# Performance work log

Hardware: AMD Instinct MI355X
Metric: run time of the kernel (lower is better)

## Reference

```python
import jax, jax.numpy as jnp
import numpy as np

EPS = 1e-3
D_MODEL = 512
SEQ = 1024
BATCH = 4
N_LAYERS = 2
N_HEAD = 8
D_HEAD = 64
D_INNER = 1024


def _position_table(n_pos, d):
    # Faithful to PositionEncoding: sin applied to even cols; the cos line in
    # the source is a no-op (missing assignment), so odd cols stay raw.
    j = np.arange(d)
    pos = np.arange(n_pos)[:, None]
    pe = pos / np.power(10000.0, 2 * (j // 2) / d)
    pe[0] = 0.0
    pe[1:, 0::2] = np.sin(pe[1:, 0::2])
    return jnp.asarray(pe, dtype=jnp.float32)


def _layer_norm(z, a, b):
    # torch.std is unbiased (ddof=1); eps added to sigma, not variance
    mu = jnp.mean(z, axis=-1, keepdims=True)
    sigma = jnp.sqrt(jnp.sum((z - mu) ** 2, axis=-1, keepdims=True) / (z.shape[-1] - 1))
    return (z - mu) / (sigma + EPS) * a + b


def setup_inputs() -> dict:
    key = jax.random.key(0)
    ks = jax.random.split(key, 10)
    s = 0.02
    return {
        "x": jax.random.normal(ks[0], (BATCH, SEQ, D_MODEL), dtype=jnp.float32),
        "pos_enc": _position_table(SEQ, D_MODEL),
        "w_qs": jax.random.normal(ks[1], (N_LAYERS, N_HEAD, D_MODEL, D_HEAD), dtype=jnp.float32) * s,
        "w_ks": jax.random.normal(ks[2], (N_LAYERS, N_HEAD, D_MODEL, D_HEAD), dtype=jnp.float32) * s,
        "w_vs": jax.random.normal(ks[3], (N_LAYERS, N_HEAD, D_MODEL, D_HEAD), dtype=jnp.float32) * s,
        "ln1_a": jnp.ones((N_LAYERS, D_MODEL), dtype=jnp.float32),
        "ln1_b": jnp.zeros((N_LAYERS, D_MODEL), dtype=jnp.float32),
        "w1": jax.random.normal(ks[4], (N_LAYERS, D_INNER, D_MODEL), dtype=jnp.float32) * s,
        "b1": jax.random.normal(ks[5], (N_LAYERS, D_INNER), dtype=jnp.float32) * s,
        "w2": jax.random.normal(ks[6], (N_LAYERS, D_MODEL, D_INNER), dtype=jnp.float32) * s,
        "b2": jax.random.normal(ks[7], (N_LAYERS, D_MODEL), dtype=jnp.float32) * s,
        "ln2_a": jnp.ones((N_LAYERS, D_MODEL), dtype=jnp.float32),
        "ln2_b": jnp.zeros((N_LAYERS, D_MODEL), dtype=jnp.float32),
    }


def reference(x, pos_enc, w_qs, w_ks, w_vs, ln1_a, ln1_b, w1, b1, w2, b2, ln2_a, ln2_b):
    temper = jnp.sqrt(jnp.float32(D_MODEL))  # scale uses d_model, not d_k (as in source)
    x = x + pos_enc[None, :, :]
    for i in range(N_LAYERS):
        residual = x
        # per-head projections: [h, b, l, dk]
        q = jnp.einsum('bld,hdk->hblk', x, w_qs[i])
        k = jnp.einsum('bld,hdk->hblk', x, w_ks[i])
        v = jnp.einsum('bld,hdv->hblv', x, w_vs[i])
        attn = jax.nn.softmax(jnp.einsum('hbqk,hbmk->hbqm', q, k) / temper, axis=-1)
        out = jnp.einsum('hbqm,hbmv->hbqv', attn, v)
        # permute(1,2,0,3): concat heads along feature dim -> [b, l, h*dv]
        out = out.transpose(1, 2, 0, 3).reshape(BATCH, SEQ, N_HEAD * D_HEAD)
        x = _layer_norm(out + residual, ln1_a[i], ln1_b[i])
        # positionwise FFN (1x1 convs == linears)
        h = jax.nn.relu(jnp.einsum('bld,fd->blf', x, w1[i]) + b1[i])
        o = jnp.einsum('blf,df->bld', h, w2[i]) + b2[i]
        x = _layer_norm(o + x, ln2_a[i], ln2_b[i])
    return x
```

## Files before the change

### kernel.cpp

```cpp
#include <hip/hip_runtime.h>
#include <math.h>

#define D_MODEL 512
#define SEQ     1024
#define BATCH   4
#define N_LAYERS 2
#define N_HEAD  8
#define D_HEAD  64
#define D_INNER 1024
#define NTOK    (BATCH*SEQ)
#define LN_EPS  1e-3f

typedef float f32x4 __attribute__((ext_vector_type(4)));
typedef short bf16x8 __attribute__((ext_vector_type(8)));
typedef unsigned short ushort_t;
typedef unsigned int uint_t;
typedef unsigned long long ull_t;

__device__ inline ushort_t f2bf(float f) {
    uint_t u = __float_as_uint(f);
    u += 0x7FFFu + ((u >> 16) & 1u);
    return (ushort_t)(u >> 16);
}
__device__ inline float bf2f(ushort_t h) {
    return __uint_as_float((uint_t)h << 16);
}

#define PREP_E0 (NTOK * D_MODEL)
#define PREP_E1 (1536 * 512)
#define PREP_EW (N_LAYERS * D_INNER * D_MODEL)
#define PREP_TOTAL (PREP_E0 + 2 * PREP_E1 + 2 * PREP_EW)

__global__ void prep_kernel(const float* __restrict__ x,
                            const float* __restrict__ pe,
                            const float* __restrict__ w_qs,
                            const float* __restrict__ w_ks,
                            const float* __restrict__ w_vs,
                            const float* __restrict__ w1,
                            const float* __restrict__ w2,
                            float* __restrict__ X,
                            ushort_t* __restrict__ Xraw,
                            ushort_t* __restrict__ Wqkv,
                            ushort_t* __restrict__ WqkvL,
                            ushort_t* __restrict__ W1b,
                            ushort_t* __restrict__ W2b) {
    int idx = blockIdx.x * 256 + threadIdx.x;
    if (idx < PREP_E0) {
        int l = (idx / D_MODEL) % SEQ;
        int d = idx % D_MODEL;
        float xv = x[idx];
        X[idx] = xv + pe[l * D_MODEL + d];
        Xraw[idx] = f2bf(xv);
        return;
    }
    idx -= PREP_E0;
    if (idx < 2 * PREP_E1) {
        int layer = idx / PREP_E1;
        int j = idx - layer * PREP_E1;
        int n = j >> 9, k = j & 511;
        int which = n >> 9, h = (n >> 6) & 7, d = n & 63;
        size_t wofs = (size_t)layer * N_HEAD * D_MODEL * D_HEAD;
        const float* W = (which == 0) ? w_qs + wofs
                       : (which == 1) ? w_ks + wofs : w_vs + wofs;
        float v = W[((size_t)h * D_MODEL + k) * D_HEAD + d];
        ushort_t hv = f2bf(v);
        Wqkv[(size_t)layer * PREP_E1 + j] = hv;
        if (layer == 0) WqkvL[j] = f2bf(v - bf2f(hv));
        return;
    }
    idx -= 2 * PREP_E1;
    if (idx < PREP_EW) { W1b[idx] = f2bf(w1[idx]); return; }
    idx -= PREP_EW;
    W2b[idx] = f2bf(w2[idx]);
}

__device__ inline void qkv_scatter(f32x4 a, int n, int m_base,
                                   const float* __restrict__ pew,
                                   ushort_t* Qhi, ushort_t* Qlo,
                                   ushort_t* Khi, ushort_t* Klo,
                                   ushort_t* Vt) {
    int which = n >> 9, hd = n & 511;
    int head = hd >> 6, d = hd & 63;
    int hb = head * BATCH + (m_base >> 10);
    int l  = m_base & 1023;
    if (pew) {
#pragma unroll
        for (int r = 0; r < 4; r++) a[r] += pew[(size_t)(l + r) * 1536 + n];
    }
    if (which == 2) {
        ushort4 pk = make_ushort4(f2bf(a[0]), f2bf(a[1]), f2bf(a[2]), f2bf(a[3]));
        *(ushort4*)(Vt + ((size_t)hb * D_HEAD + d) * SEQ + l) = pk;
    } else {
        ushort_t* H = (which == 0) ? Qhi : Khi;
        ushort_t* L = (which == 0) ? Qlo : Klo;
#pragma unroll
        for (int r = 0; r < 4; r++) {
            float v = a[r];
            ushort_t hv = f2bf(v);
            size_t off = ((size_t)hb * SEQ + l + r) * D_HEAD + d;
            H[off] = hv;
            L[off] = f2bf(v - bf2f(hv));
        }
    }
}

template<int MODE, int TM, int TN, int BK>
__global__ __launch_bounds__(256, 4)
void gemm_kernel(const ushort_t* __restrict__ A, const ushort_t* __restrict__ Bt,
                 const float* __restrict__ bias, const float* __restrict__ pew,
                 float* __restrict__ outF, ushort_t* __restrict__ outB,
                 ushort_t* __restrict__ Qhi, ushort_t* __restrict__ Qlo,
                 ushort_t* __restrict__ Khi, ushort_t* __restrict__ Klo,
                 ushort_t* __restrict__ Vt,
                 int M, int N, int K) {
    constexpr int WM = TM / 2, WN = TN / 2;
    constexpr int MT = WM / 16, NT = WN / 16;
    constexpr int CPR = BK / 8;
    __shared__ ushort_t As[TM][BK + 8];
    __shared__ ushort_t Bs[TN][BK + 8];
    const int tid = threadIdx.x;
    const int m0 = blockIdx.y * TM, n0 = blockIdx.x * TN;
    const int w = tid >> 6, lane = tid & 63;
    const int wr = w >> 1, wc = w & 1;
    const int col = lane & 15, quad = lane >> 4;

    f32x4 acc[MT][NT] = {};

    for (int k0 = 0; k0 < K; k0 += BK) {
        __syncthreads();
#pragma unroll
        for (int p = 0; p < TM * CPR / 256; p++) {
            int idx = p * 256 + tid;
            int row = idx / CPR, ch = (idx % CPR) * 8;
            *(uint4*)(&As[row][ch]) =
                *(const uint4*)(A + (size_t)(m0 + row) * K + k0 + ch);
        }
#pragma unroll
        for (int p = 0; p < TN * CPR / 256; p++) {
            int idx = p * 256 + tid;
            int row = idx / CPR, ch = (idx % CPR) * 8;
            *(uint4*)(&Bs[row][ch]) =
                *(const uint4*)(Bt + (size_t)(n0 + row) * K + k0 + ch);
        }
        __syncthreads();
#pragma unroll
        for (int ks = 0; ks < BK; ks += 32) {
            bf16x8 af[MT], bfr[NT];
#pragma unroll
            for (int t = 0; t < MT; t++)
                af[t] = *(const bf16x8*)(&As[wr * WM + t * 16 + col][ks + quad * 8]);
#pragma unroll
            for (int t = 0; t < NT; t++)
                bfr[t] = *(const bf16x8*)(&Bs[wc * WN + t * 16 + col][ks + quad * 8]);
#pragma unroll
            for (int mt = 0; mt < MT; mt++)
#pragma unroll
                for (int nt = 0; nt < NT; nt++)
                    acc[mt][nt] = __builtin_amdgcn_mfma_f32_16x16x32_bf16(
                        af[mt], bfr[nt], acc[mt][nt], 0, 0, 0);
        }
    }

#pragma unroll
    for (int mt = 0; mt < MT; mt++) {
#pragma unroll
        for (int nt = 0; nt < NT; nt++) {
            int n = n0 + wc * WN + nt * 16 + col;
            int m_base = m0 + wr * WM + mt * 16 + quad * 4;
            if (MODE == 0) {
                qkv_scatter(acc[mt][nt], n, m_base, pew, Qhi, Qlo, Khi, Klo, Vt);
            } else {
#pragma unroll
                for (int r = 0; r < 4; r++) {
                    int m = m_base + r;
                    float v = acc[mt][nt][r];
                    if (MODE == 1) {
                        float t = fmaxf(v + bias[n], 0.f);
                        outB[(size_t)m * N + n] = f2bf(t);
                    } else {
                        outF[(size_t)m * N + n] = v + bias[n];
                    }
                }
            }
        }
    }
}

__global__ __launch_bounds__(256, 4)
void gemm_hilo_kernel(const float* __restrict__ A,
                      const ushort_t* __restrict__ Bh,
                      const ushort_t* __restrict__ Bl,
                      float* __restrict__ outF, int M, int N, int K) {
    __shared__ ushort_t Ash[64][72];
    __shared__ ushort_t Asl[64][72];
    __shared__ ushort_t Bsh[64][72];
    __shared__ ushort_t Bsl[64][72];
    const int tid = threadIdx.x;
    const int m0 = blockIdx.y * 64, n0 = blockIdx.x * 64;
    const int w = tid >> 6, lane = tid & 63;
    const int wm = (w >> 1) * 32, wn = (w & 1) * 32;
    const int col = lane & 15, quad = lane >> 4;

    f32x4 acc[2][2] = {};

    for (int k0 = 0; k0 < K; k0 += 64) {
        __syncthreads();
#pragma unroll
        for (int p = 0; p < 4; p++) {
            int idx = p * 256 + tid;
            int row = idx >> 4, c4 = (idx & 15) * 4;
            float4 v = *(const float4*)(A + (size_t)(m0 + row) * K + k0 + c4);
            ushort_t h0 = f2bf(v.x), h1 = f2bf(v.y), h2 = f2bf(v.z), h3 = f2bf(v.w);
            *(ushort4*)(&Ash[row][c4]) = make_ushort4(h0, h1, h2, h3);
            *(ushort4*)(&Asl[row][c4]) = make_ushort4(
                f2bf(v.x - bf2f(h0)), f2bf(v.y - bf2f(h1)),
                f2bf(v.z - bf2f(h2)), f2bf(v.w - bf2f(h3)));
        }
#pragma unroll
        for (int p = 0; p < 2; p++) {
            int idx = p * 256 + tid;
            int row = idx >> 3, ch = (idx & 7) * 8;
            *(uint4*)(&Bsh[row][ch]) =
                *(const uint4*)(Bh + (size_t)(n0 + row) * K + k0 + ch);
            *(uint4*)(&Bsl[row][ch]) =
                *(const uint4*)(Bl + (size_t)(n0 + row) * K + k0 + ch);
        }
        __syncthreads();
#pragma unroll
        for (int ks = 0; ks < 64; ks += 32) {
            bf16x8 ah[2], al[2], bh[2], bl[2];
#pragma unroll
            for (int t = 0; t < 2; t++) {
                ah[t] = *(const bf16x8*)(&Ash[wm + t * 16 + col][ks + quad * 8]);
                al[t] = *(const bf16x8*)(&Asl[wm + t * 16 + col][ks + quad * 8]);
                bh[t] = *(const bf16x8*)(&Bsh[wn + t * 16 + col][ks + quad * 8]);
                bl[t] = *(const bf16x8*)(&Bsl[wn + t * 16 + col][ks + quad * 8]);
            }
#pragma unroll
            for (int mt = 0; mt < 2; mt++)
#pragma unroll
                for (int nt = 0; nt < 2; nt++) {
                    acc[mt][nt] = __builtin_amdgcn_mfma_f32_16x16x32_bf16(
                        ah[mt], bh[nt], acc[mt][nt], 0, 0, 0);
                    acc[mt][nt] = __builtin_amdgcn_mfma_f32_16x16x32_bf16(
                        ah[mt], bl[nt], acc[mt][nt], 0, 0, 0);
                    acc[mt][nt] = __builtin_amdgcn_mfma_f32_16x16x32_bf16(
                        al[mt], bh[nt], acc[mt][nt], 0, 0, 0);
                }
        }
    }

#pragma unroll
    for (int mt = 0; mt < 2; mt++)
#pragma unroll
        for (int nt = 0; nt < 2; nt++) {
            int n = n0 + wn + nt * 16 + col;
#pragma unroll
            for (int r = 0; r < 4; r++) {
                int m = m0 + wm + mt * 16 + quad * 4 + r;
                outF[(size_t)m * N + n] = acc[mt][nt][r];
            }
        }
}

template<bool HILO>
__global__ __launch_bounds__(256, 4)
void attention_kernel(const ushort_t* __restrict__ Qhi,
                      const ushort_t* __restrict__ Qlo,
                      const ushort_t* __restrict__ Khi,
                      const ushort_t* __restrict__ Klo,
                      const ushort_t* __restrict__ Vt,
                      float* __restrict__ P0,
                      float* __restrict__ P1,
                      float2* __restrict__ ML) {
    const int bid = blockIdx.x;
    const int split = bid >> 9;
    const int r9  = bid & 511;
    const int j   = r9 >> 3;
    const int hb  = (r9 & 7) * 4 + (j >> 4);
    const int qt  = j & 15;
    const int h = hb >> 2, b = hb & 3;
    const int tid = threadIdx.x;
    const int w = tid >> 6, lane = tid & 63;
    const int col = lane & 15, quad = lane >> 4;
    const size_t kbase = (size_t)hb * SEQ * D_HEAD;
    const size_t vbase = (size_t)hb * D_HEAD * SEQ;

    __shared__ ushort_t Kh[64][72];
    __shared__ ushort_t Kl[HILO ? 64 : 1][72];
    __shared__ ushort_t Vs[64][72];
    __shared__ ushort_t Pl[4][16][72];

    bf16x8 qh[2], ql[2];
    {
        const ushort_t* qp = Qhi + kbase + (size_t)(qt * 64 + w * 16 + col) * D_HEAD;
        qh[0] = *(const bf16x8*)(qp + quad * 8);
        qh[1] = *(const bf16x8*)(qp + 32 + quad * 8);
        if (HILO) {
            const ushort_t* lp = Qlo + kbase + (size_t)(qt * 64 + w * 16 + col) * D_HEAD;
            ql[0] = *(const bf16x8*)(lp + quad * 8);
            ql[1] = *(const bf16x8*)(lp + 32 + quad * 8);
        }
    }

    f32x4 acco[4] = {};
    float mrun = -1e30f, lrun = 0.f;
    const float inv_temper = 0.04419417382415922f;

    const int tbeg = split * (SEQ / 2);
    for (int t0 = tbeg; t0 < tbeg + SEQ / 2; t0 += 64) {
        __syncthreads();
#pragma unroll
        for (int p = 0; p < 2; p++) {
            int idx = p * 256 + tid;
            int row = idx >> 3, ch = (idx & 7) * 8;
            *(uint4*)(&Kh[row][ch]) =
                *(const uint4*)(Khi + kbase + (size_t)(t0 + row) * D_HEAD + ch);
            if (HILO)
                *(uint4*)(&Kl[row][ch]) =
                    *(const uint4*)(Klo + kbase + (size_t)(t0 + row) * D_HEAD + ch);
            *(uint4*)(&Vs[row][ch]) =
                *(const uint4*)(Vt + vbase + (size_t)row * SEQ + t0 + ch);
        }
        __syncthreads();

        float sc[4][4];
#pragma unroll
        for (int nt = 0; nt < 4; nt++) {
            bf16x8 kh0 = *(const bf16x8*)(&Kh[nt * 16 + col][quad * 8]);
            bf16x8 kh1 = *(const bf16x8*)(&Kh[nt * 16 + col][32 + quad * 8]);
            f32x4 s = {};
            s = __builtin_amdgcn_mfma_f32_16x16x32_bf16(kh0, qh[0], s, 0, 0, 0);
            s = __builtin_amdgcn_mfma_f32_16x16x32_bf16(kh1, qh[1], s, 0, 0, 0);
            if (HILO) {
                bf16x8 kl0 = *(const bf16x8*)(&Kl[nt * 16 + col][quad * 8]);
                bf16x8 kl1 = *(const bf16x8*)(&Kl[nt * 16 + col][32 + quad * 8]);
                s = __builtin_amdgcn_mfma_f32_16x16x32_bf16(kl0, qh[0], s, 0, 0, 0);
                s = __builtin_amdgcn_mfma_f32_16x16x32_bf16(kl1, qh[1], s, 0, 0, 0);
                s = __builtin_amdgcn_mfma_f32_16x16x32_bf16(kh0, ql[0], s, 0, 0, 0);
                s = __builtin_amdgcn_mfma_f32_16x16x32_bf16(kh1, ql[1], s, 0, 0, 0);
            }
#pragma unroll
            for (int r = 0; r < 4; r++) sc[nt][r] = s[r] * inv_temper;
        }

        bf16x8 va0[4], va1[4];
#pragma unroll
        for (int nt = 0; nt < 4; nt++) {
            va0[nt] = *(const bf16x8*)(&Vs[nt * 16 + col][quad * 8]);
            va1[nt] = *(const bf16x8*)(&Vs[nt * 16 + col][32 + quad * 8]);
        }

        float tmax = sc[0][0];
#pragma unroll
        for (int nt = 0; nt < 4; nt++)
#pragma unroll
            for (int r = 0; r < 4; r++) tmax = fmaxf(tmax, sc[nt][r]);
        tmax = fmaxf(tmax, __shfl_xor(tmax, 16, 64));
        tmax = fmaxf(tmax, __shfl_xor(tmax, 32, 64));

        float mn = fmaxf(mrun, tmax);
        float alpha = __expf(mrun - mn);
        mrun = mn;
        float tsum = 0.f;
#pragma unroll
        for (int nt = 0; nt < 4; nt++) {
            float p0 = __expf(sc[nt][0] - mn);
            float p1 = __expf(sc[nt][1] - mn);
            float p2 = __expf(sc[nt][2] - mn);
            float p3 = __expf(sc[nt][3] - mn);
            tsum += (p0 + p1) + (p2 + p3);
            ull_t pk = (ull_t)f2bf(p0) | ((ull_t)f2bf(p1) << 16)
                     | ((ull_t)f2bf(p2) << 32) | ((ull_t)f2bf(p3) << 48);
            *(ull_t*)(&Pl[w][col][nt * 16 + quad * 4]) = pk;
        }
        tsum += __shfl_xor(tsum, 16, 64);
        tsum += __shfl_xor(tsum, 32, 64);
        lrun = lrun * alpha + tsum;
#pragma unroll
        for (int nt = 0; nt < 4; nt++)
#pragma unroll
            for (int r = 0; r < 4; r++) acco[nt][r] *= alpha;

        __threadfence_block();

        union { ulong2 u; bf16x8 v; } pa0, pa1;
        pa0.u = *(const ulong2*)(&Pl[w][col][quad * 8]);
        pa1.u = *(const ulong2*)(&Pl[w][col][32 + quad * 8]);
#pragma unroll
        for (int nt = 0; nt < 4; nt++) {
            acco[nt] = __builtin_amdgcn_mfma_f32_16x16x32_bf16(va0[nt], pa0.v, acco[nt], 0, 0, 0);
            acco[nt] = __builtin_amdgcn_mfma_f32_16x16x32_bf16(va1[nt], pa1.v, acco[nt], 0, 0, 0);
        }
    }

    const int qrow = qt * 64 + w * 16 + col;
    float* dst = split ? P1 : P0;
#pragma unroll
    for (int nt = 0; nt < 4; nt++)
        *(f32x4*)(&dst[((size_t)b * SEQ + qrow) * D_MODEL + h * D_HEAD
                       + nt * 16 + quad * 4]) = acco[nt];
    if (quad == 0)
        ML[((size_t)split * 32 + hb) * SEQ + qrow] = make_float2(mrun, lrun);
}

__device__ inline float block_sum_256(float v, float* tmp) {
#pragma unroll
    for (int off = 32; off > 0; off >>= 1) v += __shfl_down(v, off, 64);
    if ((threadIdx.x & 63) == 0) tmp[threadIdx.x >> 6] = v;
    __syncthreads();
    return tmp[0] + tmp[1] + tmp[2] + tmp[3];
}

__global__ void add_norm_kernel(const float* __restrict__ A,
                                const float* __restrict__ R,
                                const float* __restrict__ ga,
                                const float* __restrict__ gb,
                                float* __restrict__ Out,
                                ushort_t* __restrict__ OutBf) {
    int tok = blockIdx.x, tid = threadIdx.x;
    __shared__ float t1[4], t2[4];
    size_t base = (size_t)tok * D_MODEL;
    float z0 = A[base + tid]       + R[base + tid];
    float z1 = A[base + tid + 256] + R[base + tid + 256];
    float s = block_sum_256(z0 + z1, t1);
    float mu = s * (1.f / (float)D_MODEL);
    float d0 = z0 - mu, d1 = z1 - mu;
    float ss = block_sum_256(d0 * d0 + d1 * d1, t2);
    float sigma = sqrtf(ss * (1.f / (float)(D_MODEL - 1)));
    float inv = 1.f / (sigma + LN_EPS);
    float r0 = d0 * inv * ga[tid]       + gb[tid];
    float r1 = d1 * inv * ga[tid + 256] + gb[tid + 256];
    Out[base + tid]         = r0;
    Out[base + tid + 256]   = r1;
    OutBf[base + tid]       = f2bf(r0);
    OutBf[base + tid + 256] = f2bf(r1);
}

__global__ void add_norm_combine_kernel(const float* __restrict__ Pa,
                                        const float* __restrict__ Pb,
                                        const float2* __restrict__ ML,
                                        const float* __restrict__ R,
                                        const float* __restrict__ ga,
                                        const float* __restrict__ gb,
                                        float* __restrict__ Out,
                                        ushort_t* __restrict__ OutBf) {
    int tok = blockIdx.x, tid = threadIdx.x;
    int b = tok >> 10, l = tok & 1023;
    __shared__ float t1[4], t2[4];
    int h0 = tid >> 6;
    float s0a, s0b, s1a, s1b;
    {
        int hb0 = h0 * 4 + b;
        float2 u0 = ML[(size_t)hb0 * SEQ + l];
        float2 u1 = ML[(size_t)(32 + hb0) * SEQ + l];
        float M = fmaxf(u0.x, u1.x);
        float e0 = __expf(u0.x - M), e1 = __expf(u1.x - M);
        float inv = 1.f / (e0 * u0.y + e1 * u1.y);
        s0a = e0 * inv; s0b = e1 * inv;
        int hb1 = (h0 + 4) * 4 + b;
        float2 v0 = ML[(size_t)hb1 * SEQ + l];
        float2 v1 = ML[(size_t)(32 + hb1) * SEQ + l];
        float M2 = fmaxf(v0.x, v1.x);
        float f0 = __expf(v0.x - M2), f1 = __expf(v1.x - M2);
        float inv2 = 1.f / (f0 * v0.y + f1 * v1.y);
        s1a = f0 * inv2; s1b = f1 * inv2;
    }
    size_t base = (size_t)tok * D_MODEL;
    float z0 = Pa[base + tid] * s0a + Pb[base + tid] * s0b + R[base + tid];
    float z1 = Pa[base + tid + 256] * s1a + Pb[base + tid + 256] * s1b
             + R[base + tid + 256];
    float s = block_sum_256(z0 + z1, t1);
    float mu = s * (1.f / (float)D_MODEL);
    float d0 = z0 - mu, d1 = z1 - mu;
    float ss = block_sum_256(d0 * d0 + d1 * d1, t2);
    float sigma = sqrtf(ss * (1.f / (float)(D_MODEL - 1)));
    float inv = 1.f / (sigma + LN_EPS);
    float r0 = d0 * inv * ga[tid]       + gb[tid];
    float r1 = d1 * inv * ga[tid + 256] + gb[tid + 256];
    Out[base + tid]         = r0;
    Out[base + tid + 256]   = r1;
    OutBf[base + tid]       = f2bf(r0);
    OutBf[base + tid + 256] = f2bf(r1);
}

extern "C" void kernel_launch(void* const* d_in, const int* in_sizes, int n_in,
                              void* d_out, int out_size, void* d_ws, size_t ws_size,
                              hipStream_t stream) {
    const float* x     = (const float*)d_in[0];
    const float* pe    = (const float*)d_in[1];
    const float* w_qs  = (const float*)d_in[2];
    const float* w_ks  = (const float*)d_in[3];
    const float* w_vs  = (const float*)d_in[4];
    const float* ln1_a = (const float*)d_in[5];
    const float* ln1_b = (const float*)d_in[6];
    const float* w1    = (const float*)d_in[7];
    const float* b1    = (const float*)d_in[8];
    const float* w2    = (const float*)d_in[9];
    const float* b2    = (const float*)d_in[10];
    const float* ln2_a = (const float*)d_in[11];
    const float* ln2_b = (const float*)d_in[12];
    float* out = (float*)d_out;

    const size_t NXD = (size_t)NTOK * D_MODEL;
    char* p = (char*)d_ws;
    float*    X    = (float*)p;     p += NXD * 4;
    float*    Ob   = (float*)p;     p += NXD * 4;
    ushort_t* Xbf  = (ushort_t*)p;  p += NXD * 2;
    ushort_t* Xraw = (ushort_t*)p;  p += NXD * 2;
    ushort_t* Qhi  = (ushort_t*)p;  p += NXD * 2;
    ushort_t* Qlo  = (ushort_t*)p;  p += NXD * 2;
    ushort_t* Khi  = (ushort_t*)p;  p += NXD * 2;
    ushort_t* Klo  = (ushort_t*)p;  p += NXD * 2;
    ushort_t* Vt   = (ushort_t*)p;  p += NXD * 2;
    ushort_t* Wqkv = (ushort_t*)p;  p += (size_t)N_LAYERS * 1536 * 512 * 2;
    ushort_t* WqkvL= (ushort_t*)p;  p += (size_t)1536 * 512 * 2;
    ushort_t* W1b  = (ushort_t*)p;  p += (size_t)N_LAYERS * D_INNER * D_MODEL * 2;
    ushort_t* W2b  = (ushort_t*)p;  p += (size_t)N_LAYERS * D_MODEL * D_INNER * 2;
    float2*   ML   = (float2*)p;
    ushort_t* Hbf  = Qhi;
    float*    PEW  = Ob;

    prep_kernel<<<(PREP_TOTAL + 255) / 256, 256, 0, stream>>>(
        x, pe, w_qs, w_ks, w_vs, w1, w2, X, Xraw, Wqkv, WqkvL, W1b, W2b);

    for (int i = 0; i < N_LAYERS; i++) {
        if (i == 0) {
            gemm_hilo_kernel<<<dim3(1536 / 64, SEQ / 64), 256, 0, stream>>>(
                pe, Wqkv, WqkvL, PEW, SEQ, 1536, D_MODEL);
            gemm_kernel<0, 64, 64, 128><<<dim3(1536 / 64, NTOK / 64), 256, 0, stream>>>(
                Xraw, Wqkv, nullptr, PEW, nullptr, nullptr,
                Qhi, Qlo, Khi, Klo, Vt, NTOK, 1536, D_MODEL);
            attention_kernel<true><<<1024, 256, 0, stream>>>(
                Qhi, Qlo, Khi, Klo, Vt, Ob, out, ML);
        } else {
            gemm_kernel<0, 64, 64, 128><<<dim3(1536 / 64, NTOK / 64), 256, 0, stream>>>(
                Xbf, Wqkv + (size_t)i * 1536 * 512, nullptr, nullptr, nullptr,
                nullptr, Qhi, Qlo, Khi, Klo, Vt, NTOK, 1536, D_MODEL);
            attention_kernel<false><<<1024, 256, 0, stream>>>(
                Qhi, Qlo, Khi, Klo, Vt, Ob, out, ML);
        }

        add_norm_combine_kernel<<<NTOK, 256, 0, stream>>>(
            Ob, out, ML, X, ln1_a + i * D_MODEL, ln1_b + i * D_MODEL, X, Xbf);

        gemm_kernel<1, 64, 64, 128><<<dim3(D_INNER / 64, NTOK / 64), 256, 0, stream>>>(
            Xbf, W1b + (size_t)i * D_INNER * D_MODEL, b1 + (size_t)i * D_INNER,
            nullptr, nullptr, Hbf, nullptr, nullptr, nullptr, nullptr, nullptr,
            NTOK, D_INNER, D_MODEL);

        gemm_kernel<2, 64, 64, 128><<<dim3(D_MODEL / 64, NTOK / 64), 256, 0, stream>>>(
            Hbf, W2b + (size_t)i * D_MODEL * D_INNER, b2 + (size_t)i * D_MODEL,
            nullptr, Ob, nullptr, nullptr, nullptr, nullptr, nullptr, nullptr,
            NTOK, D_MODEL, D_INNER);

        float* dst = (i == N_LAYERS - 1) ? out : X;
        add_norm_kernel<<<NTOK, 256, 0, stream>>>(
            Ob, X, ln2_a + i * D_MODEL, ln2_b + i * D_MODEL, dst, Xbf);
    }
}
```

Before: 287.1 us.

## Load GEMM tiles directly to LDS with XOR swizzle and larger tiles

Replaces the register-staged global-to-shared copies in the bf16 MFMA GEMM with global_load_lds direct-to-LDS loads. Shared memory is laid out with an XOR-swizzled chunk layout in place of padding, so fragment reads avoid bank conflicts. The QKV and FFN1 GEMMs switch from 64x64x128 tiles to 128x128x64 tiles, with launch bounds lowered for the larger tile. This aims to cut VGPR staging and load latency and to raise per-block data reuse, at the cost of fewer blocks and lower occupancy. FFN2 keeps the smaller tile.

Measured after the change: 295.5 us. +2.9%, slower.

```diff
diff --git a/kernel.cpp b/kernel.cpp
--- a/kernel.cpp
+++ b/kernel.cpp
@@ -24,6 +24,12 @@
 }
 __device__ inline float bf2f(ushort_t h) {
     return __uint_as_float((uint_t)h << 16);
+}
+
+__device__ __forceinline__ void gload16(const ushort_t* g, ushort_t* l) {
+    __builtin_amdgcn_global_load_lds(
+        (const __attribute__((address_space(1))) void*)g,
+        (__attribute__((address_space(3))) void*)l, 16, 0, 0);
 }
 
 #define PREP_E0 (NTOK * D_MODEL)
@@ -105,7 +111,7 @@
 }
 
 template<int MODE, int TM, int TN, int BK>
-__global__ __launch_bounds__(256, 4)
+__global__ __launch_bounds__(256, (TM == 128 ? 2 : 4))
 void gemm_kernel(const ushort_t* __restrict__ A, const ushort_t* __restrict__ Bt,
                  const float* __restrict__ bias, const float* __restrict__ pew,
                  float* __restrict__ outF, ushort_t* __restrict__ outB,
@@ -116,42 +122,49 @@
     constexpr int WM = TM / 2, WN = TN / 2;
     constexpr int MT = WM / 16, NT = WN / 16;
     constexpr int CPR = BK / 8;
-    __shared__ ushort_t As[TM][BK + 8];
-    __shared__ ushort_t Bs[TN][BK + 8];
+    constexpr int RPW = 512 / BK;
+    constexpr int WPTA = TM / RPW / 4;
+    constexpr int WPTB = TN / RPW / 4;
+    __shared__ ushort_t As[TM * BK];
+    __shared__ ushort_t Bs[TN * BK];
     const int tid = threadIdx.x;
     const int m0 = blockIdx.y * TM, n0 = blockIdx.x * TN;
     const int w = tid >> 6, lane = tid & 63;
     const int wr = w >> 1, wc = w & 1;
     const int col = lane & 15, quad = lane >> 4;
+    const int lr = lane / CPR;
+    const int lc = lane % CPR;
 
     f32x4 acc[MT][NT] = {};
 
     for (int k0 = 0; k0 < K; k0 += BK) {
         __syncthreads();
 #pragma unroll
-        for (int p = 0; p < TM * CPR / 256; p++) {
-            int idx = p * 256 + tid;
-            int row = idx / CPR, ch = (idx % CPR) * 8;
-            *(uint4*)(&As[row][ch]) =
-                *(const uint4*)(A + (size_t)(m0 + row) * K + k0 + ch);
-        }
-#pragma unroll
-        for (int p = 0; p < TN * CPR / 256; p++) {
-            int idx = p * 256 + tid;
-            int row = idx / CPR, ch = (idx % CPR) * 8;
-            *(uint4*)(&Bs[row][ch]) =
-                *(const uint4*)(Bt + (size_t)(n0 + row) * K + k0 + ch);
+        for (int wi = 0; wi < WPTA; wi++) {
+            int row = (w * WPTA + wi) * RPW + lr;
+            int sch = lc ^ (row & 7);
+            gload16(A + (size_t)(m0 + row) * K + k0 + sch * 8,
+                    &As[(w * WPTA + wi) * RPW * BK]);
+        }
+#pragma unroll
+        for (int wi = 0; wi < WPTB; wi++) {
+            int row = (w * WPTB + wi) * RPW + lr;
+            int sch = lc ^ (row & 7);
+            gload16(Bt + (size_t)(n0 + row) * K + k0 + sch * 8,
+                    &Bs[(w * WPTB + wi) * RPW * BK]);
         }
         __syncthreads();
 #pragma unroll
         for (int ks = 0; ks < BK; ks += 32) {
+            const int cb = ks >> 3;
+            const int sc_ = ((cb + quad) ^ (col & 7)) * 8;
             bf16x8 af[MT], bfr[NT];
 #pragma unroll
             for (int t = 0; t < MT; t++)
-                af[t] = *(const bf16x8*)(&As[wr * WM + t * 16 + col][ks + quad * 8]);
+                af[t] = *(const bf16x8*)(&As[(wr * WM + t * 16 + col) * BK + sc_]);
 #pragma unroll
             for (int t = 0; t < NT; t++)
-                bfr[t] = *(const bf16x8*)(&Bs[wc * WN + t * 16 + col][ks + quad * 8]);
+                bfr[t] = *(const bf16x8*)(&Bs[(wc * WN + t * 16 + col) * BK + sc_]);
 #pragma unroll
             for (int mt = 0; mt < MT; mt++)
 #pragma unroll
@@ -528,13 +541,13 @@
         if (i == 0) {
             gemm_hilo_kernel<<<dim3(1536 / 64, SEQ / 64), 256, 0, stream>>>(
                 pe, Wqkv, WqkvL, PEW, SEQ, 1536, D_MODEL);
-            gemm_kernel<0, 64, 64, 128><<<dim3(1536 / 64, NTOK / 64), 256, 0, stream>>>(
+            gemm_kernel<0, 128, 128, 64><<<dim3(1536 / 128, NTOK / 128), 256, 0, stream>>>(
                 Xraw, Wqkv, nullptr, PEW, nullptr, nullptr,
                 Qhi, Qlo, Khi, Klo, Vt, NTOK, 1536, D_MODEL);
             attention_kernel<true><<<1024, 256, 0, stream>>>(
                 Qhi, Qlo, Khi, Klo, Vt, Ob, out, ML);
         } else {
-            gemm_kernel<0, 64, 64, 128><<<dim3(1536 / 64, NTOK / 64), 256, 0, stream>>>(
+            gemm_kernel<0, 128, 128, 64><<<dim3(1536 / 128, NTOK / 128), 256, 0, stream>>>(
                 Xbf, Wqkv + (size_t)i * 1536 * 512, nullptr, nullptr, nullptr,
                 nullptr, Qhi, Qlo, Khi, Klo, Vt, NTOK, 1536, D_MODEL);
             attention_kernel<false><<<1024, 256, 0, stream>>>(
@@ -544,7 +557,7 @@
         add_norm_combine_kernel<<<NTOK, 256, 0, stream>>>(
             Ob, out, ML, X, ln1_a + i * D_MODEL, ln1_b + i * D_MODEL, X, Xbf);
 
-        gemm_kernel<1, 64, 64, 128><<<dim3(D_INNER / 64, NTOK / 64), 256, 0, stream>>>(
+        gemm_kernel<1, 128, 128, 64><<<dim3(D_INNER / 128, NTOK / 128), 256, 0, stream>>>(
             Xbf, W1b + (size_t)i * D_INNER * D_MODEL, b1 + (size_t)i * D_INNER,
             nullptr, nullptr, Hbf, nullptr, nullptr, nullptr, nullptr, nullptr,
             NTOK, D_INNER, D_MODEL);
```
